# Kernel optimization log

Hardware: AMD Instinct MI355X
Metric: run time of the kernel (lower is better)

Reference implementation:

```python
import jax, jax.numpy as jnp
import numpy as np

B, S, D, H = 8, 2048, 1024, 16
HD = D // H  # head_dim = 64


def setup_inputs() -> dict:
    key = jax.random.key(0)
    ks = jax.random.split(key, 10)
    s = 0.02
    return {
        "x": jax.random.normal(ks[0], (B, S, D), jnp.float32),
        "mask": jnp.zeros((B, 1, S), jnp.float32),
        "Wq": jax.random.normal(ks[1], (D, D), jnp.float32) * s,
        "bq": jnp.zeros((D,), jnp.float32),
        "Wk": jax.random.normal(ks[2], (D, D), jnp.float32) * s,
        "bk": jnp.zeros((D,), jnp.float32),
        "Wv": jax.random.normal(ks[3], (D, D), jnp.float32) * s,
        "bv": jnp.zeros((D,), jnp.float32),
        "wa": jax.random.normal(ks[4], (HD, 1), jnp.float32) * s,
        "ba": jnp.zeros((1,), jnp.float32),
        "wb": jax.random.normal(ks[5], (HD, 1), jnp.float32) * s,
        "bb": jnp.zeros((1,), jnp.float32),
        "Wu": jax.random.normal(ks[6], (HD, HD), jnp.float32) * s,
        "bu": jnp.zeros((HD,), jnp.float32),
        "Wo": jax.random.normal(ks[7], (D, D), jnp.float32) * s,
        "bo": jnp.zeros((D,), jnp.float32),
        "gamma": jnp.ones((D,), jnp.float32),
        "beta_ln": jnp.zeros((D,), jnp.float32),
    }


def _split_heads(t):
    # [B,S,D] -> [B,H,S,HD]
    return t.reshape(B, S, H, HD).transpose(0, 2, 1, 3)


def reference(x, mask, Wq, bq, Wk, bk, Wv, bv, wa, ba, wb, bb, Wu, bu, Wo, bo, gamma, beta_ln):
    scale = 1.0 / jnp.sqrt(jnp.float32(HD))
    q = _split_heads(x @ Wq + bq)  # [B,H,S,HD]
    k = _split_heads(x @ Wk + bk)
    v = _split_heads(x @ Wv + bv)

    # additive attention over queries -> global query vector per head
    alphascore = (jnp.squeeze(q @ wa, -1) + ba[0]) * scale + mask  # [B,H,S]
    alphaw = jax.nn.softmax(alphascore, axis=-1)
    q_av = jnp.einsum('bhs,bhsd->bhd', alphaw, q)

    p = k * q_av[:, :, None, :]  # gated keys [B,H,S,HD]
    betascore = (jnp.squeeze(p @ wb, -1) + bb[0]) * scale + mask
    betaw = jax.nn.softmax(betascore, axis=-1)
    p_av = jnp.einsum('bhs,bhsd->bhd', betaw, p)

    u = v * p_av[:, :, None, :]  # gated values
    r = u @ Wu + bu  # [B,H,S,HD]
    newr = (r + q).transpose(0, 2, 1, 3).reshape(B, S, D)
    attn_out = newr @ Wo + bo

    h = x + attn_out
    mu = jnp.mean(h, axis=-1, keepdims=True)
    var = jnp.mean(jnp.square(h - mu), axis=-1, keepdims=True)
    return (h - mu) * jax.lax.rsqrt(var + 1e-6) * gamma + beta_ln
```

## Files before the change

### kernel.cpp

```cpp
#include <hip/hip_runtime.h>
#include <cstdint>

#define BB 8
#define SS 2048
#define DD 1024
#define HH 16
#define HDIM 64
#define MTOT (BB*SS)
#define NQKV 3072

typedef __attribute__((ext_vector_type(8))) __bf16 bf16x8;
typedef __attribute__((ext_vector_type(4))) float f32x4;

#define AS1(p) ((const __attribute__((address_space(1))) void*)(p))
#define AS3(p) ((__attribute__((address_space(3))) void*)(p))

__device__ __forceinline__ float bf2f(uint16_t u){
  return __uint_as_float(((uint32_t)u) << 16);
}
__device__ __forceinline__ uint16_t f2bf(float f){
  uint32_t u = __float_as_uint(f);
  return (uint16_t)((u + 0x7fffu + ((u >> 16) & 1u)) >> 16);
}

__global__ __launch_bounds__(256)
void k_prep(const float* __restrict__ x,
            const float* __restrict__ Wq, const float* __restrict__ Wk,
            const float* __restrict__ Wv, const float* __restrict__ Wo,
            const float* __restrict__ bq, const float* __restrict__ bk,
            const float* __restrict__ bv,
            uint16_t* __restrict__ xb, uint16_t* __restrict__ Wt,
            uint16_t* __restrict__ WoT, float* __restrict__ bqkv)
{
  __shared__ float t[32][33];
  const int blk = blockIdx.x, tid = threadIdx.x;
  if (blk < 2048){
    const int n4 = MTOT*DD/4;
    for (int i = blk*256 + tid; i < n4; i += 2048*256){
      float4 v = reinterpret_cast<const float4*>(x)[i];
      ushort4 o;
      o.x = f2bf(v.x); o.y = f2bf(v.y); o.z = f2bf(v.z); o.w = f2bf(v.w);
      reinterpret_cast<ushort4*>(xb)[i] = o;
    }
  } else if (blk < 6144){
    const int zb = blk - 2048;
    const int z = zb >> 10, rem = zb & 1023;
    const int by = rem >> 5, bx = rem & 31;
    const float* src = (z==0)?Wq:(z==1)?Wk:(z==2)?Wv:Wo;
    uint16_t* dst = (z<3) ? (Wt + (size_t)z*1024*1024) : WoT;
    const int k0 = by*32, n0 = bx*32;
    const int tx = tid & 31, ty = tid >> 5;
    #pragma unroll
    for (int r = 0; r < 4; ++r)
      t[ty + r*8][tx] = src[(size_t)(k0 + ty + r*8)*1024 + n0 + tx];
    __syncthreads();
    #pragma unroll
    for (int r = 0; r < 4; ++r)
      dst[(size_t)(n0 + ty + r*8)*1024 + k0 + tx] = f2bf(t[tx][ty + r*8]);
  } else {
    const int i = (blk - 6144)*256 + tid;
    if (i < NQKV)
      bqkv[i] = (i < 1024) ? bq[i] : (i < 2048) ? bk[i-1024] : bv[i-2048];
  }
}


#define BARRIER __builtin_amdgcn_s_barrier()

#define READA(BUF, MH) { \
  const uint16_t* _sl = lds + ((BUF)*4 + (MH))*8192; \
  _Pragma("unroll") \
  for (int f = 0; f < 4; ++f) \
    _Pragma("unroll") \
    for (int ks = 0; ks < 2; ++ks) \
      a[f][ks] = *(const bf16x8*)(_sl + (wm*64 + f*16 + l15)*64 + (((ks*4 + l4) ^ l7)<<3)); \
}

#define READB(BUF, NH, BV) { \
  const uint16_t* _sl = lds + ((BUF)*4 + 2 + (NH))*8192; \
  _Pragma("unroll") \
  for (int j = 0; j < 2; ++j) \
    _Pragma("unroll") \
    for (int ks = 0; ks < 2; ++ks) \
      BV[j][ks] = *(const bf16x8*)(_sl + (wn*32 + j*16 + l15)*64 + (((ks*4 + l4) ^ l7)<<3)); \
}

#define MMA(MH, NH, BV) { \
  __builtin_amdgcn_s_setprio(1); \
  _Pragma("unroll") \
  for (int ks = 0; ks < 2; ++ks) \
    _Pragma("unroll") \
    for (int f = 0; f < 4; ++f) \
      _Pragma("unroll") \
      for (int j = 0; j < 2; ++j) \
        acc[(MH)*4+f][(NH)*2+j] = __builtin_amdgcn_mfma_f32_16x16x32_bf16(a[f][ks], BV[j][ks], acc[(MH)*4+f][(NH)*2+j], 0, 0, 0); \
  __builtin_amdgcn_s_setprio(0); }

#define STAGEA(T, H) { \
  char* _d = (char*)lds + ((((T)&1)*4 + (H))*16384) + wave*1024; \
  _Pragma("unroll") \
  for (int l = 0; l < 2; ++l) \
    __builtin_amdgcn_global_load_lds(AS1(pA + (l*131072 + (H)*65536 + (T)*64)), AS3(_d + l*8192), 16, 0, 0); \
}

#define STAGEB(T, H) { \
  char* _d = (char*)lds + ((((T)&1)*4 + 2 + (H))*16384) + wave*1024; \
  _Pragma("unroll") \
  for (int l = 0; l < 2; ++l) \
    __builtin_amdgcn_global_load_lds(AS1(pB + (l*131072 + (H)*32768 + (T)*64)), AS3(_d + l*8192), 16, 0, 0); \
}

template<int EPI, int NB_T>
__global__ __launch_bounds__(512)
void k_gemm256(const uint16_t* __restrict__ A, const uint16_t* __restrict__ Bt,
               const float* __restrict__ bias, const uint16_t* __restrict__ resid16,
               uint16_t* __restrict__ Cout)
{
  constexpr int N = NB_T * 256;
  __shared__ uint16_t lds[8 * 8192];
  const int tid = threadIdx.x;
  const int lane = tid & 63, wave = tid >> 6;
  const int wm = wave >> 2, wn = wave & 3;
  const int l15 = lane & 15, l4 = lane >> 4, l7 = lane & 7;

  const int nwg = gridDim.x, cpx = nwg >> 3, bid = blockIdx.x;
  const int wg = (bid & 7) * cpx + (bid >> 3);
  const int m0 = (wg / NB_T) << 8, n0 = (wg % NB_T) << 8;

  const int colbase = (((tid & 7) ^ ((tid >> 3) & 7)) << 3);
  const uint16_t* pA = A  + (size_t)(m0 + (tid >> 3)) * 1024 + colbase;
  const uint16_t* pB = Bt + (size_t)(n0 + ((tid >> 8) << 6) + ((tid >> 3) & 31)) * 1024 + colbase;

  f32x4 acc[8][4] = {};
  bf16x8 a[4][2], b0[2][2], b1[2][2];

  STAGEA(0,0); STAGEB(0,1); STAGEA(0,1); STAGEB(0,0);
  STAGEA(1,0); STAGEB(1,1); STAGEA(1,1);
  asm volatile("s_waitcnt vmcnt(6)" ::: "memory");
  BARRIER;

  #pragma unroll
  for (int I = 0; I < 7; ++I){
    const int e = 2*I;
    READA(0,0); READB(0,0,b0); STAGEB(e+1, 0);
    BARRIER; MMA(0,0,b0); BARRIER;
    READB(0,1,b1); STAGEA(e+2, 0);
    BARRIER; MMA(0,1,b1); BARRIER;
    READA(0,1); STAGEB(e+2, 1);
    BARRIER; MMA(1,1,b1); BARRIER;
    STAGEA(e+2, 1);
    asm volatile("s_waitcnt vmcnt(6)" ::: "memory");
    BARRIER; MMA(1,0,b0); BARRIER;
    READA(1,0); READB(1,0,b0); STAGEB(e+2, 0);
    BARRIER; MMA(0,0,b0); BARRIER;
    READB(1,1,b1); STAGEA(e+3, 0);
    BARRIER; MMA(0,1,b1); BARRIER;
    READA(1,1); STAGEB(e+3, 1);
    BARRIER; MMA(1,1,b1); BARRIER;
    STAGEA(e+3, 1);
    asm volatile("s_waitcnt vmcnt(6)" ::: "memory");
    BARRIER; MMA(1,0,b0); BARRIER;
  }

  {
    READA(0,0); READB(0,0,b0); STAGEB(15, 0);
    BARRIER; MMA(0,0,b0); BARRIER;
    READB(0,1,b1);
    BARRIER; MMA(0,1,b1); BARRIER;
    READA(0,1);
    BARRIER; MMA(1,1,b1); BARRIER;
    asm volatile("s_waitcnt vmcnt(0)" ::: "memory");
    BARRIER; MMA(1,0,b0); BARRIER;
    READA(1,0); READB(1,0,b0);
    BARRIER; MMA(0,0,b0); BARRIER;
    READB(1,1,b1);
    BARRIER; MMA(0,1,b1); BARRIER;
    READA(1,1);
    BARRIER; MMA(1,1,b1); BARRIER;
    MMA(1,0,b0);
  }

  #pragma unroll
  for (int mh = 0; mh < 2; ++mh)
  #pragma unroll
  for (int f = 0; f < 4; ++f)
  #pragma unroll
  for (int nh = 0; nh < 2; ++nh)
  #pragma unroll
  for (int j = 0; j < 2; ++j){
    const int gcol = n0 + wn*64 + nh*32 + j*16 + l15;
    const float bi = bias[gcol];
    const int rbase = m0 + wm*128 + mh*64 + f*16 + l4*4;
    #pragma unroll
    for (int rr = 0; rr < 4; ++rr){
      const size_t idx = (size_t)(rbase + rr)*N + gcol;
      float v = acc[mh*4+f][nh*2+j][rr] + bi;
      if (EPI == 1) v += bf2f(resid16[idx]);
      Cout[idx] = f2bf(v);
    }
  }
}

__device__ __forceinline__ float block_red_max512(float v, float* red, int tid){
  red[tid] = v; __syncthreads();
  for (int off = 256; off > 0; off >>= 1){
    if (tid < off) red[tid] = fmaxf(red[tid], red[tid+off]);
    __syncthreads();
  }
  float r = red[0]; __syncthreads();
  return r;
}
__device__ __forceinline__ float block_red_sum512(float v, float* red, int tid){
  red[tid] = v; __syncthreads();
  for (int off = 256; off > 0; off >>= 1){
    if (tid < off) red[tid] += red[tid+off];
    __syncthreads();
  }
  float r = red[0]; __syncthreads();
  return r;
}

__device__ __forceinline__ void pool_pass(
    const uint16_t* __restrict__ base, const float* __restrict__ mrow,
    const float* __restrict__ wv, float biasv,
    uint16_t* qlds, float* sc, float* red, float (*part)[64],
    float* ca, float* scal, int tid, int wave, int lane)
{
  if (tid < 64) ca[tid] = 0.f;
  if (tid == 0){ scal[0] = -3.4e38f; scal[1] = 0.f; }
  __syncthreads();
  #pragma unroll
  for (int c = 0; c < 2; ++c){
    {
      const int r8 = lane >> 3, sl = lane & 7;
      #pragma unroll
      for (int it = 0; it < 16; ++it){
        const int rowg = c*1024 + (wave*16 + it)*8 + r8;
        const uint16_t* src = base + (size_t)rowg*NQKV + ((sl ^ r8) << 3);
        __builtin_amdgcn_global_load_lds(AS1(src),
            AS3((char*)qlds + (wave*16 + it)*1024), 16, 0, 0);
      }
    }
    asm volatile("s_waitcnt vmcnt(0)" ::: "memory");
    __syncthreads();
    #pragma unroll
    for (int rr = 0; rr < 2; ++rr){
      const int row = tid + rr*512;
      float acc = 0.f;
      #pragma unroll
      for (int jj = 0; jj < 8; ++jj){
        bf16x8 v = *(const bf16x8*)(qlds + row*64 + ((jj ^ (row & 7)) << 3));
        #pragma unroll
        for (int e = 0; e < 8; ++e) acc += (float)v[e] * wv[jj*8 + e];
      }
      sc[row] = (acc + biasv)*0.125f + mrow[c*1024 + row];
    }
    __syncthreads();
    const float lm = fmaxf(sc[tid], sc[tid+512]);
    const float mx = block_red_max512(lm, red, tid);
    const float e0 = __expf(sc[tid] - mx), e1 = __expf(sc[tid+512] - mx);
    sc[tid] = e0; sc[tid+512] = e1;
    const float lc = block_red_sum512(e0 + e1, red, tid);
    {
      const int j = tid & 63, g = tid >> 6;
      const int slot_sh = j >> 3, jin = j & 7;
      float a = 0.f;
      for (int s = 0; s < 128; ++s){
        const int row = g*128 + s;
        a += sc[row] * bf2f(qlds[row*64 + (((slot_sh) ^ (row & 7)) << 3) + jin]);
      }
      part[g][j] = a;
    }
    __syncthreads();
    if (tid < 64){
      float colc = 0.f;
      #pragma unroll
      for (int g2 = 0; g2 < 8; ++g2) colc += part[g2][tid];
      const float m_old = scal[0], l_old = scal[1];
      const float m_new = fmaxf(m_old, mx);
      const float fo = __expf(m_old - m_new), fc = __expf(mx - m_new);
      ca[tid] = ca[tid]*fo + colc*fc;
      if (tid == 0){ scal[1] = l_old*fo + lc*fc; scal[0] = m_new; }
    }
    __syncthreads();
  }
}

__global__ __launch_bounds__(512)
void k_head(const uint16_t* __restrict__ qkv, const float* __restrict__ mask,
            const float* __restrict__ wa, const float* __restrict__ ba,
            const float* __restrict__ wb, const float* __restrict__ bbp,
            const float* __restrict__ Wu, uint16_t* __restrict__ WuPT)
{
  __shared__ uint16_t qlds[1024*64];
  __shared__ float sc[1024];
  __shared__ float red[512];
  __shared__ float part[8][64];
  __shared__ float ca[64];
  __shared__ float qav[64], wvec[64], wva[64], pav[64];
  __shared__ float scal[2];

  const int bh = blockIdx.x, b = bh >> 4, h = bh & 15;
  const int tid = threadIdx.x, wave = tid >> 6, lane = tid & 63;
  const uint16_t* qb  = qkv + (size_t)b*SS*NQKV + h*64;
  const uint16_t* kb2 = qb + 1024;
  const float* mrow = mask + b*SS;

  if (tid < 64) wva[tid] = wa[tid];
  __syncthreads();

  pool_pass(qb, mrow, wva, ba[0], qlds, sc, red, part, ca, scal, tid, wave, lane);
  if (tid < 64){
    const float qv = ca[tid] / scal[1];
    qav[tid] = qv;
    wvec[tid] = qv * wb[tid];
  }
  __syncthreads();

  pool_pass(kb2, mrow, wvec, bbp[0], qlds, sc, red, part, ca, scal, tid, wave, lane);
  if (tid < 64) pav[tid] = qav[tid] * (ca[tid] / scal[1]);
  __syncthreads();

  uint16_t* dst = WuPT + (size_t)bh*4096;
  for (int idx = tid; idx < 4096; idx += 512){
    const int i = idx & 63, jcol = idx >> 6;
    dst[idx] = f2bf(pav[i]*Wu[i*64 + jcol]);
  }
}

__global__ __launch_bounds__(256)
void k_newr(const uint16_t* __restrict__ qkv, const uint16_t* __restrict__ WuPT,
            const float* __restrict__ bu, uint16_t* __restrict__ newr)
{
  const int bh = blockIdx.x >> 3, st = blockIdx.x & 7;
  const int b = bh >> 4, h = bh & 15;
  const int tid = threadIdx.x, wave = tid >> 6, lane = tid & 63;
  const int l15 = lane & 15, l4 = lane >> 4;
  const int s0 = st*256 + wave*64;
  const uint16_t* vb = qkv + 2048 + h*64;
  const uint16_t* wt = WuPT + (size_t)bh*4096;

  f32x4 acc[4][4] = {};
  #pragma unroll
  for (int ks = 0; ks < 2; ++ks){
    bf16x8 bfr[4];
    #pragma unroll
    for (int n = 0; n < 4; ++n)
      bfr[n] = *(const bf16x8*)(wt + (n*16 + l15)*64 + ks*32 + l4*8);
    #pragma unroll
    for (int m = 0; m < 4; ++m){
      const int s = s0 + m*16 + l15;
      bf16x8 af = *(const bf16x8*)(vb + (size_t)(b*SS + s)*NQKV + ks*32 + l4*8);
      #pragma unroll
      for (int n = 0; n < 4; ++n)
        acc[m][n] = __builtin_amdgcn_mfma_f32_16x16x32_bf16(af, bfr[n], acc[m][n], 0, 0, 0);
    }
  }
  #pragma unroll
  for (int n = 0; n < 4; ++n){
    const int j = n*16 + l15;
    const float bj = bu[j];
    #pragma unroll
    for (int m = 0; m < 4; ++m){
      #pragma unroll
      for (int r = 0; r < 4; ++r){
        const int s = s0 + m*16 + l4*4 + r;
        const size_t qidx = (size_t)(b*SS + s)*NQKV + h*64 + j;
        const float q = bf2f(qkv[qidx]);
        newr[(size_t)(b*SS + s)*DD + h*64 + j] = f2bf(acc[m][n][r] + bj + q);
      }
    }
  }
}

__global__ __launch_bounds__(256)
void k_ln(const uint16_t* __restrict__ h16, const float* __restrict__ gamma,
          const float* __restrict__ beta, float* __restrict__ out)
{
  __shared__ float r1[256], r2[256];
  const int row = blockIdx.x, tid = threadIdx.x;
  const ushort4 hv = ((const ushort4*)(h16 + (size_t)row*DD))[tid];
  float v0 = bf2f(hv.x), v1 = bf2f(hv.y), v2 = bf2f(hv.z), v3 = bf2f(hv.w);
  float s  = v0 + v1 + v2 + v3;
  float ss = v0*v0 + v1*v1 + v2*v2 + v3*v3;
  r1[tid] = s; r2[tid] = ss; __syncthreads();
  for (int off = 128; off > 0; off >>= 1){
    if (tid < off){ r1[tid] += r1[tid+off]; r2[tid] += r2[tid+off]; }
    __syncthreads();
  }
  const float mu  = r1[0]*(1.f/1024.f);
  const float var = r2[0]*(1.f/1024.f) - mu*mu;
  const float inv = rsqrtf(var + 1e-6f);
  const float4 g  = ((const float4*)gamma)[tid];
  const float4 be = ((const float4*)beta)[tid];
  float4 o;
  o.x = (v0-mu)*inv*g.x + be.x;
  o.y = (v1-mu)*inv*g.y + be.y;
  o.z = (v2-mu)*inv*g.z + be.z;
  o.w = (v3-mu)*inv*g.w + be.w;
  ((float4*)(out + (size_t)row*DD))[tid] = o;
}

extern "C" void kernel_launch(void* const* d_in, const int* in_sizes, int n_in,
                              void* d_out, int out_size, void* d_ws, size_t ws_size,
                              hipStream_t stream) {
  const float* x    = (const float*)d_in[0];
  const float* mask = (const float*)d_in[1];
  const float* Wq   = (const float*)d_in[2];
  const float* bq   = (const float*)d_in[3];
  const float* Wk   = (const float*)d_in[4];
  const float* bk   = (const float*)d_in[5];
  const float* Wv   = (const float*)d_in[6];
  const float* bv   = (const float*)d_in[7];
  const float* wa   = (const float*)d_in[8];
  const float* ba   = (const float*)d_in[9];
  const float* wb   = (const float*)d_in[10];
  const float* bb   = (const float*)d_in[11];
  const float* Wu   = (const float*)d_in[12];
  const float* bu   = (const float*)d_in[13];
  const float* Wo   = (const float*)d_in[14];
  const float* bo   = (const float*)d_in[15];
  const float* gamma= (const float*)d_in[16];
  const float* beta = (const float*)d_in[17];
  float* out = (float*)d_out;

  char* ws = (char*)d_ws;
  const size_t MB = 1ull << 20;
  uint16_t* xb    = (uint16_t*)(ws);
  uint16_t* Wt    = (uint16_t*)(ws + 32*MB);
  uint16_t* WoT   = (uint16_t*)(ws + 38*MB);
  float*    bqkv  = (float*)   (ws + 40*MB);
  uint16_t* WuPT  = (uint16_t*)(ws + 41*MB);
  uint16_t* qkv   = (uint16_t*)(ws + 42*MB);
  uint16_t* newr  = (uint16_t*)(ws + 138*MB);
  uint16_t* hbuf16= (uint16_t*)(ws + 42*MB);

  k_prep<<<6156, 256, 0, stream>>>(x, Wq, Wk, Wv, Wo, bq, bk, bv, xb, Wt, WoT, bqkv);

  k_gemm256<0,12><<<(MTOT/256)*(NQKV/256), 512, 0, stream>>>(xb, Wt, bqkv, nullptr, qkv);
  k_head<<<BB*HH, 512, 0, stream>>>(qkv, mask, wa, ba, wb, bb, Wu, WuPT);
  k_newr<<<BB*HH*8, 256, 0, stream>>>(qkv, WuPT, bu, newr);
  k_gemm256<1,4><<<(MTOT/256)*(DD/256), 512, 0, stream>>>(newr, WoT, bo, xb, hbuf16);
  k_ln<<<MTOT, 256, 0, stream>>>(hbuf16, gamma, beta, out);
}
```

Baseline: 229.8 us.

## Split per-head pooling into grid-wide partial-sum kernels with separate merge passes

Replaces the single 128-block k_head kernel, which ran both softmax pooling passes serially per head, with a four-kernel pipeline: pool, mergeA, pool, mergeB. Each pool kernel uses 2048 blocks that each cover 8 rows across all heads and write per-block partial numerators and denominators. The merge kernels then reduce these to the pooled query vector, and finally to pav and the scaled Wu matrix. The aim is to fill the whole GPU instead of 128 blocks and to drop the per-chunk block-wide reductions. The cost is extra launches, extra global traffic for the partial buffers, and exponentials computed without subtracting the running max, which could overflow on large scores.

Result: slower. 238.0 us (+3.5%).

```diff
diff --git a/kernel.cpp b/kernel.cpp
--- a/kernel.cpp
+++ b/kernel.cpp
@@ -63,7 +63,6 @@
       bqkv[i] = (i < 1024) ? bq[i] : (i < 2048) ? bk[i-1024] : bv[i-2048];
   }
 }
-
 
 #define BARRIER __builtin_amdgcn_s_barrier()
 
@@ -201,128 +200,106 @@
   }
 }
 
-__device__ __forceinline__ float block_red_max512(float v, float* red, int tid){
-  red[tid] = v; __syncthreads();
-  for (int off = 256; off > 0; off >>= 1){
-    if (tid < off) red[tid] = fmaxf(red[tid], red[tid+off]);
+template<int PASS>
+__global__ __launch_bounds__(256)
+void k_pool(const uint16_t* __restrict__ qkv, const float* __restrict__ mask,
+            const float* __restrict__ w64, const float* __restrict__ biasp,
+            const float* __restrict__ wvecB,
+            float* __restrict__ cpart, float* __restrict__ dpart)
+{
+  __shared__ float probe[1024];
+  const int blk = blockIdx.x, tid = threadIdx.x, lane = tid & 63;
+  const int r0 = blk*8, b = r0 >> 11;
+  #pragma unroll
+  for (int k2 = 0; k2 < 4; ++k2){
+    const int c = k2*256 + tid;
+    probe[c] = (PASS == 0) ? w64[c & 63] : wvecB[b*1024 + c];
+  }
+  __syncthreads();
+  const float bias = biasp[0];
+  const uint16_t* base = qkv + (PASS == 0 ? 0 : 1024);
+  const int c0 = tid*4;
+  const float p0 = probe[c0], p1 = probe[c0+1], p2 = probe[c0+2], p3 = probe[c0+3];
+  float r0a = 0.f, r1a = 0.f, r2a = 0.f, r3a = 0.f, dsum = 0.f;
+  #pragma unroll
+  for (int r = 0; r < 8; ++r){
+    const int row = r0 + r;
+    const ushort4 raw = *(const ushort4*)(base + (size_t)row*NQKV + c0);
+    const float v0 = bf2f(raw.x), v1 = bf2f(raw.y), v2 = bf2f(raw.z), v3 = bf2f(raw.w);
+    float s = v0*p0 + v1*p1 + v2*p2 + v3*p3;
+    s += __shfl_xor(s, 1); s += __shfl_xor(s, 2);
+    s += __shfl_xor(s, 4); s += __shfl_xor(s, 8);
+    const float E = __expf((s + bias)*0.125f + mask[row]);
+    r0a += v0*E; r1a += v1*E; r2a += v2*E; r3a += v3*E;
+    dsum += E;
+  }
+  float* cp = cpart + (size_t)blk*1024 + c0;
+  cp[0] = r0a; cp[1] = r1a; cp[2] = r2a; cp[3] = r3a;
+  if ((lane & 15) == 0) dpart[blk*16 + (tid >> 4)] = dsum;
+}
+
+__global__ __launch_bounds__(256)
+void k_mergeA(const float* __restrict__ cpart, const float* __restrict__ dpart,
+              const float* __restrict__ wb,
+              float* __restrict__ qavB, float* __restrict__ wvecB)
+{
+  __shared__ float red[8][32];
+  __shared__ float dred[256];
+  const int blk = blockIdx.x, tid = threadIdx.x;
+  const int b = blk >> 5, ch = blk & 31;
+  const int c = ch*32 + (tid & 31), pg = tid >> 5;
+  const int h = ch >> 1;
+  float s = 0.f;
+  #pragma unroll
+  for (int p = 0; p < 32; ++p)
+    s += cpart[(size_t)(b*256 + pg*32 + p)*1024 + c];
+  red[pg][tid & 31] = s;
+  dred[tid] = dpart[(b*256 + tid)*16 + h];
+  __syncthreads();
+  for (int off = 128; off > 0; off >>= 1){
+    if (tid < off) dred[tid] += dred[tid + off];
     __syncthreads();
   }
-  float r = red[0]; __syncthreads();
-  return r;
-}
-__device__ __forceinline__ float block_red_sum512(float v, float* red, int tid){
-  red[tid] = v; __syncthreads();
-  for (int off = 256; off > 0; off >>= 1){
-    if (tid < off) red[tid] += red[tid+off];
+  if (tid < 32){
+    float cs = 0.f;
+    #pragma unroll
+    for (int g = 0; g < 8; ++g) cs += red[g][tid];
+    const int col = ch*32 + tid;
+    const float qv = cs / dred[0];
+    qavB[b*1024 + col]  = qv;
+    wvecB[b*1024 + col] = qv * wb[col & 63];
+  }
+}
+
+__global__ __launch_bounds__(256)
+void k_mergeB(const float* __restrict__ cpart, const float* __restrict__ dpart,
+              const float* __restrict__ qavB, const float* __restrict__ Wu,
+              uint16_t* __restrict__ WuPT)
+{
+  __shared__ float red[4][64];
+  __shared__ float dred[256];
+  __shared__ float pav[64];
+  const int bh = blockIdx.x, b = bh >> 4, h = bh & 15;
+  const int tid = threadIdx.x;
+  const int j = tid & 63, pg = tid >> 6;
+  float s = 0.f;
+  #pragma unroll
+  for (int p = 0; p < 64; ++p)
+    s += cpart[(size_t)(b*256 + pg*64 + p)*1024 + h*64 + j];
+  red[pg][j] = s;
+  dred[tid] = dpart[(b*256 + tid)*16 + h];
+  __syncthreads();
+  for (int off = 128; off > 0; off >>= 1){
+    if (tid < off) dred[tid] += dred[tid + off];
     __syncthreads();
   }
-  float r = red[0]; __syncthreads();
-  return r;
-}
-
-__device__ __forceinline__ void pool_pass(
-    const uint16_t* __restrict__ base, const float* __restrict__ mrow,
-    const float* __restrict__ wv, float biasv,
-    uint16_t* qlds, float* sc, float* red, float (*part)[64],
-    float* ca, float* scal, int tid, int wave, int lane)
-{
-  if (tid < 64) ca[tid] = 0.f;
-  if (tid == 0){ scal[0] = -3.4e38f; scal[1] = 0.f; }
+  if (tid < 64){
+    const float cs = red[0][tid] + red[1][tid] + red[2][tid] + red[3][tid];
+    pav[tid] = qavB[b*1024 + h*64 + tid] * (cs / dred[0]);
+  }
   __syncthreads();
-  #pragma unroll
-  for (int c = 0; c < 2; ++c){
-    {
-      const int r8 = lane >> 3, sl = lane & 7;
-      #pragma unroll
-      for (int it = 0; it < 16; ++it){
-        const int rowg = c*1024 + (wave*16 + it)*8 + r8;
-        const uint16_t* src = base + (size_t)rowg*NQKV + ((sl ^ r8) << 3);
-        __builtin_amdgcn_global_load_lds(AS1(src),
-            AS3((char*)qlds + (wave*16 + it)*1024), 16, 0, 0);
-      }
-    }
-    asm volatile("s_waitcnt vmcnt(0)" ::: "memory");
-    __syncthreads();
-    #pragma unroll
-    for (int rr = 0; rr < 2; ++rr){
-      const int row = tid + rr*512;
-      float acc = 0.f;
-      #pragma unroll
-      for (int jj = 0; jj < 8; ++jj){
-        bf16x8 v = *(const bf16x8*)(qlds + row*64 + ((jj ^ (row & 7)) << 3));
-        #pragma unroll
-        for (int e = 0; e < 8; ++e) acc += (float)v[e] * wv[jj*8 + e];
-      }
-      sc[row] = (acc + biasv)*0.125f + mrow[c*1024 + row];
-    }
-    __syncthreads();
-    const float lm = fmaxf(sc[tid], sc[tid+512]);
-    const float mx = block_red_max512(lm, red, tid);
-    const float e0 = __expf(sc[tid] - mx), e1 = __expf(sc[tid+512] - mx);
-    sc[tid] = e0; sc[tid+512] = e1;
-    const float lc = block_red_sum512(e0 + e1, red, tid);
-    {
-      const int j = tid & 63, g = tid >> 6;
-      const int slot_sh = j >> 3, jin = j & 7;
-      float a = 0.f;
-      for (int s = 0; s < 128; ++s){
-        const int row = g*128 + s;
-        a += sc[row] * bf2f(qlds[row*64 + (((slot_sh) ^ (row & 7)) << 3) + jin]);
-      }
-      part[g][j] = a;
-    }
-    __syncthreads();
-    if (tid < 64){
-      float colc = 0.f;
-      #pragma unroll
-      for (int g2 = 0; g2 < 8; ++g2) colc += part[g2][tid];
-      const float m_old = scal[0], l_old = scal[1];
-      const float m_new = fmaxf(m_old, mx);
-      const float fo = __expf(m_old - m_new), fc = __expf(mx - m_new);
-      ca[tid] = ca[tid]*fo + colc*fc;
-      if (tid == 0){ scal[1] = l_old*fo + lc*fc; scal[0] = m_new; }
-    }
-    __syncthreads();
-  }
-}
-
-__global__ __launch_bounds__(512)
-void k_head(const uint16_t* __restrict__ qkv, const float* __restrict__ mask,
-            const float* __restrict__ wa, const float* __restrict__ ba,
-            const float* __restrict__ wb, const float* __restrict__ bbp,
-            const float* __restrict__ Wu, uint16_t* __restrict__ WuPT)
-{
-  __shared__ uint16_t qlds[1024*64];
-  __shared__ float sc[1024];
-  __shared__ float red[512];
-  __shared__ float part[8][64];
-  __shared__ float ca[64];
-  __shared__ float qav[64], wvec[64], wva[64], pav[64];
-  __shared__ float scal[2];
-
-  const int bh = blockIdx.x, b = bh >> 4, h = bh & 15;
-  const int tid = threadIdx.x, wave = tid >> 6, lane = tid & 63;
-  const uint16_t* qb  = qkv + (size_t)b*SS*NQKV + h*64;
-  const uint16_t* kb2 = qb + 1024;
-  const float* mrow = mask + b*SS;
-
-  if (tid < 64) wva[tid] = wa[tid];
-  __syncthreads();
-
-  pool_pass(qb, mrow, wva, ba[0], qlds, sc, red, part, ca, scal, tid, wave, lane);
-  if (tid < 64){
-    const float qv = ca[tid] / scal[1];
-    qav[tid] = qv;
-    wvec[tid] = qv * wb[tid];
-  }
-  __syncthreads();
-
-  pool_pass(kb2, mrow, wvec, bbp[0], qlds, sc, red, part, ca, scal, tid, wave, lane);
-  if (tid < 64) pav[tid] = qav[tid] * (ca[tid] / scal[1]);
-  __syncthreads();
-
   uint16_t* dst = WuPT + (size_t)bh*4096;
-  for (int idx = tid; idx < 4096; idx += 512){
+  for (int idx = tid; idx < 4096; idx += 256){
     const int i = idx & 63, jcol = idx >> 6;
     dst[idx] = f2bf(pav[i]*Wu[i*64 + jcol]);
   }
@@ -434,11 +411,20 @@
   uint16_t* qkv   = (uint16_t*)(ws + 42*MB);
   uint16_t* newr  = (uint16_t*)(ws + 138*MB);
   uint16_t* hbuf16= (uint16_t*)(ws + 42*MB);
+  float* cpart = (float*)(ws + 138*MB);
+  float* dpart = (float*)(ws + 146*MB);
+  float* qavB  = (float*)(ws + 147*MB);
+  float* wvecB = (float*)(ws + 148*MB);
 
   k_prep<<<6156, 256, 0, stream>>>(x, Wq, Wk, Wv, Wo, bq, bk, bv, xb, Wt, WoT, bqkv);
 
   k_gemm256<0,12><<<(MTOT/256)*(NQKV/256), 512, 0, stream>>>(xb, Wt, bqkv, nullptr, qkv);
-  k_head<<<BB*HH, 512, 0, stream>>>(qkv, mask, wa, ba, wb, bb, Wu, WuPT);
+
+  k_pool<0><<<2048, 256, 0, stream>>>(qkv, mask, wa, ba, nullptr, cpart, dpart);
+  k_mergeA<<<256, 256, 0, stream>>>(cpart, dpart, wb, qavB, wvecB);
+  k_pool<1><<<2048, 256, 0, stream>>>(qkv, mask, nullptr, bb, wvecB, cpart, dpart);
+  k_mergeB<<<128, 256, 0, stream>>>(cpart, dpart, qavB, Wu, WuPT);
+
   k_newr<<<BB*HH*8, 256, 0, stream>>>(qkv, WuPT, bu, newr);
   k_gemm256<1,4><<<(MTOT/256)*(DD/256), 512, 0, stream>>>(newr, WoT, bo, xb, hbuf16);
   k_ln<<<MTOT, 256, 0, stream>>>(hbuf16, gamma, beta, out);
```
